# Optimization experiments

Measured on AMD Instinct MI355X. Metric: run time of the kernel, lower is better.

The kernel has to match this reference:

```python
import jax, jax.numpy as jnp
import numpy as np

NEG_BIG = -9e15
ALPHA = 0.2  # leakyrelu slope


def setup_inputs() -> dict:
    key = jax.random.key(0)
    k1, k2, k3, k4 = jax.random.split(key, 4)
    N, Fin, Fout = 8192, 256, 256
    input = jax.random.normal(k1, (N, Fin), dtype=jnp.float32)
    adj = jax.random.randint(k2, (N, N), 0, 2, dtype=jnp.int32)
    W = jax.random.normal(k3, (Fin, Fout), dtype=jnp.float32) * (1.0 / np.sqrt(Fin))
    a = jax.random.normal(k4, (2 * Fout, 1), dtype=jnp.float32) * (1.0 / np.sqrt(Fout))
    return {"input": input, "adj": adj, "W": W, "a": a}


def reference(input, adj, W, a):
    # h: [N, F]
    h = input @ W
    Fout = h.shape[1]
    # Fused score: e_ij = leakyrelu(h_i . a[:F] + h_j . a[F:])
    s1 = h @ a[:Fout, 0]   # [N]
    s2 = h @ a[Fout:, 0]   # [N]
    e = s1[:, None] + s2[None, :]            # [N, N]
    e = jnp.where(e >= 0, e, ALPHA * e)      # leaky relu
    e = jnp.where(adj > 0, e, NEG_BIG)       # mask
    attention = jax.nn.softmax(e, axis=1)    # row softmax
    h_prime = attention @ h                  # [N, F]
    return jax.nn.elu(h_prime)               # concat=True -> elu
```

## Files before the change

### kernel.cpp

```cpp
#include <hip/hip_runtime.h>
#include <hip/hip_bf16.h>

#define LRALPHA 0.2f

typedef __attribute__((ext_vector_type(8))) short frag_ab;
typedef __attribute__((ext_vector_type(4))) float frag_cd;
typedef int   iv4 __attribute__((ext_vector_type(4)));
typedef float fv4 __attribute__((ext_vector_type(4)));
typedef unsigned int uv4 __attribute__((ext_vector_type(4)));

static __device__ __forceinline__ unsigned short f2bf(float f) {
  __hip_bfloat16 b = __float2bfloat16(f);
  unsigned short u;
  __builtin_memcpy(&u, &b, 2);
  return u;
}

static __device__ __forceinline__ uv4 make_w(const iv4* ca, const fv4* cv,
                                             float s1r, float mr, float& zloc) {
  alignas(16) unsigned short wv[8];
#pragma unroll
  for (int g = 0; g < 2; ++g) {
#pragma unroll
    for (int e = 0; e < 4; ++e) {
      float ee = s1r + cv[g][e];
      ee = fmaxf(ee, LRALPHA * ee);
      float w = __expf(ee - mr);
      w = ca[g][e] ? w : 0.f;
      unsigned b = __float_as_uint(w);
      b += 0x7FFFu + ((b >> 16) & 1u);
      const unsigned short u = (unsigned short)(b >> 16);
      wv[g * 4 + e] = u;
      zloc += __uint_as_float((unsigned)u << 16);
    }
  }
  return *(const uv4*)wv;
}

__global__ __launch_bounds__(256, 4) void gat_hproj(
    const float* __restrict__ X, const float* __restrict__ W,
    const float* __restrict__ avec,
    float* __restrict__ s1, float* __restrict__ s2,
    unsigned short* __restrict__ hT) {
  const int tid = threadIdx.x;
  const int row0 = blockIdx.x * 16;
  const float* Xb = X + (size_t)row0 * 256;
  const int c = tid;

  float acc[16];
#pragma unroll
  for (int r = 0; r < 16; ++r) acc[r] = 0.f;

  for (int k = 0; k < 256; k += 4) {
    const float w0 = W[(k + 0) * 256 + c];
    const float w1 = W[(k + 1) * 256 + c];
    const float w2 = W[(k + 2) * 256 + c];
    const float w3 = W[(k + 3) * 256 + c];
#pragma unroll
    for (int r = 0; r < 16; ++r) {
      acc[r] = fmaf(Xb[r * 256 + k + 0], w0, acc[r]);
      acc[r] = fmaf(Xb[r * 256 + k + 1], w1, acc[r]);
      acc[r] = fmaf(Xb[r * 256 + k + 2], w2, acc[r]);
      acc[r] = fmaf(Xb[r * 256 + k + 3], w3, acc[r]);
    }
  }

  alignas(16) unsigned short hu[16];
#pragma unroll
  for (int r = 0; r < 16; ++r) hu[r] = f2bf(acc[r]);
  uv4* hdst = (uv4*)(hT + (size_t)c * 8192 + row0);
  hdst[0] = *(const uv4*)&hu[0];
  hdst[1] = *(const uv4*)&hu[8];

  const float a1c = avec[c];
  const float a2c = avec[256 + c];
  const int lane = tid & 63, wave = tid >> 6;
  __shared__ float r1[4][16], r2[4][16];
#pragma unroll
  for (int r = 0; r < 16; ++r) {
    float v1 = acc[r] * a1c;
    float v2 = acc[r] * a2c;
#pragma unroll
    for (int off = 32; off > 0; off >>= 1) {
      v1 += __shfl_down(v1, off);
      v2 += __shfl_down(v2, off);
    }
    if (lane == 0) { r1[wave][r] = v1; r2[wave][r] = v2; }
  }
  __syncthreads();
  if (tid < 16) {
    s1[row0 + tid] = r1[0][tid] + r1[1][tid] + r1[2][tid] + r1[3][tid];
    s2[row0 + tid] = r2[0][tid] + r2[1][tid] + r2[2][tid] + r2[3][tid];
  }
}

__global__ void gat_s2max(const float* __restrict__ s2, float* __restrict__ s2max) {
  const int tid = threadIdx.x;
  float m = -1e30f;
  for (int i = tid; i < 8192; i += 256) m = fmaxf(m, s2[i]);
#pragma unroll
  for (int off = 32; off > 0; off >>= 1) m = fmaxf(m, __shfl_down(m, off));
  __shared__ float ws[4];
  if ((tid & 63) == 0) ws[tid >> 6] = m;
  __syncthreads();
  if (tid == 0) s2max[0] = fmaxf(fmaxf(ws[0], ws[1]), fmaxf(ws[2], ws[3]));
}

__global__ __launch_bounds__(512, 4) void gat_attn(
    const int* __restrict__ adj, const unsigned short* __restrict__ hT,
    const float* __restrict__ s1, const float* __restrict__ s2,
    const float* __restrict__ s2maxp,
    float* __restrict__ pacc, float* __restrict__ pZ) {
  const int bid = blockIdx.x;
  const int x = bid & 7;
  const int ks = x >> 1;
  const int rb = ((bid >> 3) << 1) | (x & 1);
  const int row0 = rb * 64;
  const int jlo = ks * 2048;
  const int tid = threadIdx.x;
  const int wave = tid >> 6, lane = tid & 63;
  const int ln16 = lane & 15, quad = lane >> 4;

  __shared__ __align__(16) unsigned short P[2][64][72];
  __shared__ float Zred[64][8];

  const int r = tid >> 3, cq = tid & 7;
  const float s1r = s1[row0 + r];
  const float s2m = s2maxp[0];
  const float tmv = s1r + s2m;
  const float mr = tmv >= 0.f ? tmv : LRALPHA * tmv;

  const int* adjRow = adj + (size_t)(row0 + r) * 8192 + jlo + cq * 8;
  const float* s2p = s2 + jlo + cq * 8;

  frag_cd acc[4][2];
  const frag_cd fz = {0.f, 0.f, 0.f, 0.f};
#pragma unroll
  for (int mi = 0; mi < 4; ++mi)
#pragma unroll
    for (int ni = 0; ni < 2; ++ni) acc[mi][ni] = fz;

  float zloc = 0.f;
  const int NIT = 2048 / 64;

  {
    iv4 ca[2]; fv4 cv[2];
    ca[0] = __builtin_nontemporal_load((const iv4*)(adjRow));
    ca[1] = __builtin_nontemporal_load((const iv4*)(adjRow + 4));
    cv[0] = *(const fv4*)(s2p);
    cv[1] = *(const fv4*)(s2p + 4);
    *(uv4*)&P[0][r][cq * 8] = make_w(ca, cv, s1r, mr, zloc);
  }
  iv4 a[2]; fv4 v[2];
  a[0] = __builtin_nontemporal_load((const iv4*)(adjRow + 64));
  a[1] = __builtin_nontemporal_load((const iv4*)(adjRow + 68));
  v[0] = *(const fv4*)(s2p + 64);
  v[1] = *(const fv4*)(s2p + 68);
  __syncthreads();

  for (int jt = 0; jt < NIT; ++jt) {
    const int cur = jt & 1, nxt = cur ^ 1;
    const size_t jbase = (size_t)(jlo + jt * 64);

    frag_ab bf[2][2];
#pragma unroll
    for (int kk = 0; kk < 2; ++kk)
#pragma unroll
      for (int ni = 0; ni < 2; ++ni) {
        const int f = wave * 32 + ni * 16 + ln16;
        bf[kk][ni] = *(const frag_ab*)(hT + (size_t)f * 8192 + jbase + kk * 32 + quad * 8);
      }

    iv4 a2[2]; fv4 v2[2];
    if (jt + 2 < NIT) {
      const int o = (jt + 2) * 64;
      a2[0] = __builtin_nontemporal_load((const iv4*)(adjRow + o));
      a2[1] = __builtin_nontemporal_load((const iv4*)(adjRow + o + 4));
      v2[0] = *(const fv4*)(s2p + o);
      v2[1] = *(const fv4*)(s2p + o + 4);
    }

    if (jt + 1 < NIT) {
      *(uv4*)&P[nxt][r][cq * 8] = make_w(a, v, s1r, mr, zloc);
    }

#pragma unroll
    for (int kk = 0; kk < 2; ++kk) {
      frag_ab af[4];
#pragma unroll
      for (int mi = 0; mi < 4; ++mi)
        af[mi] = *(const frag_ab*)&P[cur][mi * 16 + ln16][kk * 32 + quad * 8];
#pragma unroll
      for (int mi = 0; mi < 4; ++mi)
#pragma unroll
        for (int ni = 0; ni < 2; ++ni)
          acc[mi][ni] = __builtin_amdgcn_mfma_f32_16x16x32_bf16(
              af[mi], bf[kk][ni], acc[mi][ni], 0, 0, 0);
    }
    __syncthreads();
    a[0] = a2[0]; a[1] = a2[1]; v[0] = v2[0]; v[1] = v2[1];
  }

  Zred[r][cq] = zloc;
  __syncthreads();
  if (tid < 64) {
    float z = 0.f;
#pragma unroll
    for (int q = 0; q < 8; ++q) z += Zred[tid][q];
    pZ[ks * 8192 + row0 + tid] = z;
  }

  float* paccb = pacc + ((size_t)ks * 8192 + row0) * 256;
#pragma unroll
  for (int mi = 0; mi < 4; ++mi) {
#pragma unroll
    for (int ni = 0; ni < 2; ++ni) {
      const int f = wave * 32 + ni * 16 + ln16;
#pragma unroll
      for (int reg = 0; reg < 4; ++reg) {
        const int grow = mi * 16 + quad * 4 + reg;
        __builtin_nontemporal_store(acc[mi][ni][reg], paccb + (size_t)grow * 256 + f);
      }
    }
  }
}

__global__ __launch_bounds__(256) void gat_combine(
    const float* __restrict__ pacc, const float* __restrict__ pZ,
    float* __restrict__ out) {
  const int idx = blockIdx.x * 256 + threadIdx.x;
  const int row = idx >> 6;
  const float z = pZ[row] + pZ[8192 + row] + pZ[16384 + row] + pZ[24576 + row];
  const float invz = 1.f / z;
  const size_t PSTRIDE = (size_t)8192 * 256;
  const fv4 n0 = *(const fv4*)(pacc + (size_t)idx * 4);
  const fv4 n1 = *(const fv4*)(pacc + PSTRIDE + (size_t)idx * 4);
  const fv4 n2 = *(const fv4*)(pacc + 2 * PSTRIDE + (size_t)idx * 4);
  const fv4 n3 = *(const fv4*)(pacc + 3 * PSTRIDE + (size_t)idx * 4);
  fv4 o;
#pragma unroll
  for (int e = 0; e < 4; ++e) {
    const float vsum = (n0[e] + n1[e]) + (n2[e] + n3[e]);
    const float vv = vsum * invz;
    o[e] = vv > 0.f ? vv : expm1f(vv);
  }
  *(fv4*)(out + (size_t)idx * 4) = o;
}

extern "C" void kernel_launch(void* const* d_in, const int* in_sizes, int n_in,
                              void* d_out, int out_size, void* d_ws, size_t ws_size,
                              hipStream_t stream) {
  const float* X = (const float*)d_in[0];
  const int* adj = (const int*)d_in[1];
  const float* W = (const float*)d_in[2];
  const float* avec = (const float*)d_in[3];
  float* out = (float*)d_out;

  float* wsf = (float*)d_ws;
  float* s1 = wsf;
  float* s2 = wsf + 8192;
  float* s2m = wsf + 16384;
  float* pZ = wsf + 24576;
  float* pacc = wsf + 65536;
  unsigned short* hT = (unsigned short*)(wsf + 65536 + 4 * 8192 * 256);

  hipLaunchKernelGGL(gat_hproj, dim3(512), dim3(256), 0, stream, X, W, avec, s1, s2, hT);
  hipLaunchKernelGGL(gat_s2max, dim3(1), dim3(256), 0, stream, s2, s2m);
  hipLaunchKernelGGL(gat_attn, dim3(512), dim3(512), 0, stream, adj, hT, s1, s2, s2m, pacc, pZ);
  hipLaunchKernelGGL(gat_combine, dim3(2048), dim3(256), 0, stream, pacc, pZ, out);
}
```

Measured before the change: 487.0 us.

## Fuse s2 max into projection via atomicMax and streamline softmax weight computation

Drops the separate single-block s2max kernel. The projection kernel now publishes each block's s2 maximum through an order-preserving unsigned key and atomicMax. The attention weight generation switches to exp2 with log2e-prescaled constants and packs bf16 by truncation using v_perm instead of round-to-nearest. The projection GEMM uses packed float2 FMAs, and s2 loads move later to cut live registers. Risks: the atomic key is never reset, so it relies on the workspace's initial or stale contents, and truncation changes the rounding of the attention weights.

```diff
diff --git a/kernel.cpp b/kernel.cpp
--- a/kernel.cpp
+++ b/kernel.cpp
@@ -2,11 +2,13 @@
 #include <hip/hip_bf16.h>
 
 #define LRALPHA 0.2f
+#define LOG2E 1.4426950408889634f
 
 typedef __attribute__((ext_vector_type(8))) short frag_ab;
 typedef __attribute__((ext_vector_type(4))) float frag_cd;
 typedef int   iv4 __attribute__((ext_vector_type(4)));
 typedef float fv4 __attribute__((ext_vector_type(4)));
+typedef float fv2 __attribute__((ext_vector_type(2)));
 typedef unsigned int uv4 __attribute__((ext_vector_type(4)));
 
 static __device__ __forceinline__ unsigned short f2bf(float f) {
@@ -17,57 +19,65 @@
 }
 
 static __device__ __forceinline__ uv4 make_w(const iv4* ca, const fv4* cv,
-                                             float s1r, float mr, float& zloc) {
-  alignas(16) unsigned short wv[8];
+                                             float c1, float c2, float& zloc) {
+  uv4 out;
 #pragma unroll
   for (int g = 0; g < 2; ++g) {
 #pragma unroll
-    for (int e = 0; e < 4; ++e) {
-      float ee = s1r + cv[g][e];
-      ee = fmaxf(ee, LRALPHA * ee);
-      float w = __expf(ee - mr);
-      w = ca[g][e] ? w : 0.f;
-      unsigned b = __float_as_uint(w);
-      b += 0x7FFFu + ((b >> 16) & 1u);
-      const unsigned short u = (unsigned short)(b >> 16);
-      wv[g * 4 + e] = u;
-      zloc += __uint_as_float((unsigned)u << 16);
-    }
-  }
-  return *(const uv4*)wv;
+    for (int h = 0; h < 2; ++h) {
+      unsigned b0, b1;
+#pragma unroll
+      for (int e = 0; e < 2; ++e) {
+        const int idx = h * 2 + e;
+        const float u = fmaf(cv[g][idx], LOG2E, c1);
+        const float m = fmaxf(u, LRALPHA * u);
+        float w = exp2f(m - c2);
+        w = ca[g][idx] ? w : 0.f;
+        const unsigned bb = __float_as_uint(w);
+        zloc += __uint_as_float(bb & 0xFFFF0000u);
+        if (e == 0) b0 = bb; else b1 = bb;
+      }
+      out[g * 2 + h] = __builtin_amdgcn_perm(b1, b0, 0x07060302u);
+    }
+  }
+  return out;
 }
 
 __global__ __launch_bounds__(256, 4) void gat_hproj(
     const float* __restrict__ X, const float* __restrict__ W,
     const float* __restrict__ avec,
     float* __restrict__ s1, float* __restrict__ s2,
+    unsigned* __restrict__ s2key,
     unsigned short* __restrict__ hT) {
   const int tid = threadIdx.x;
   const int row0 = blockIdx.x * 16;
   const float* Xb = X + (size_t)row0 * 256;
   const int c = tid;
 
-  float acc[16];
-#pragma unroll
-  for (int r = 0; r < 16; ++r) acc[r] = 0.f;
+  fv2 acc2[8];
+#pragma unroll
+  for (int p = 0; p < 8; ++p) acc2[p] = (fv2){0.f, 0.f};
 
   for (int k = 0; k < 256; k += 4) {
-    const float w0 = W[(k + 0) * 256 + c];
-    const float w1 = W[(k + 1) * 256 + c];
-    const float w2 = W[(k + 2) * 256 + c];
-    const float w3 = W[(k + 3) * 256 + c];
-#pragma unroll
-    for (int r = 0; r < 16; ++r) {
-      acc[r] = fmaf(Xb[r * 256 + k + 0], w0, acc[r]);
-      acc[r] = fmaf(Xb[r * 256 + k + 1], w1, acc[r]);
-      acc[r] = fmaf(Xb[r * 256 + k + 2], w2, acc[r]);
-      acc[r] = fmaf(Xb[r * 256 + k + 3], w3, acc[r]);
+    float wq[4];
+#pragma unroll
+    for (int i = 0; i < 4; ++i) wq[i] = W[(k + i) * 256 + c];
+#pragma unroll
+    for (int p = 0; p < 8; ++p) {
+      const float* xr0 = Xb + (2 * p) * 256 + k;
+      const float* xr1 = Xb + (2 * p + 1) * 256 + k;
+#pragma unroll
+      for (int i = 0; i < 4; ++i) {
+        const fv2 xv = {xr0[i], xr1[i]};
+        const fv2 wv = {wq[i], wq[i]};
+        acc2[p] += xv * wv;
+      }
     }
   }
 
   alignas(16) unsigned short hu[16];
 #pragma unroll
-  for (int r = 0; r < 16; ++r) hu[r] = f2bf(acc[r]);
+  for (int r = 0; r < 16; ++r) hu[r] = f2bf(acc2[r >> 1][r & 1]);
   uv4* hdst = (uv4*)(hT + (size_t)c * 8192 + row0);
   hdst[0] = *(const uv4*)&hu[0];
   hdst[1] = *(const uv4*)&hu[8];
@@ -78,8 +88,9 @@
   __shared__ float r1[4][16], r2[4][16];
 #pragma unroll
   for (int r = 0; r < 16; ++r) {
-    float v1 = acc[r] * a1c;
-    float v2 = acc[r] * a2c;
+    const float av = acc2[r >> 1][r & 1];
+    float v1 = av * a1c;
+    float v2 = av * a2c;
 #pragma unroll
     for (int off = 32; off > 0; off >>= 1) {
       v1 += __shfl_down(v1, off);
@@ -89,27 +100,25 @@
   }
   __syncthreads();
   if (tid < 16) {
-    s1[row0 + tid] = r1[0][tid] + r1[1][tid] + r1[2][tid] + r1[3][tid];
-    s2[row0 + tid] = r2[0][tid] + r2[1][tid] + r2[2][tid] + r2[3][tid];
-  }
-}
-
-__global__ void gat_s2max(const float* __restrict__ s2, float* __restrict__ s2max) {
-  const int tid = threadIdx.x;
-  float m = -1e30f;
-  for (int i = tid; i < 8192; i += 256) m = fmaxf(m, s2[i]);
-#pragma unroll
-  for (int off = 32; off > 0; off >>= 1) m = fmaxf(m, __shfl_down(m, off));
-  __shared__ float ws[4];
-  if ((tid & 63) == 0) ws[tid >> 6] = m;
-  __syncthreads();
-  if (tid == 0) s2max[0] = fmaxf(fmaxf(ws[0], ws[1]), fmaxf(ws[2], ws[3]));
+    const float v1 = r1[0][tid] + r1[1][tid] + r1[2][tid] + r1[3][tid];
+    const float v2 = r2[0][tid] + r2[1][tid] + r2[2][tid] + r2[3][tid];
+    s1[row0 + tid] = v1;
+    s2[row0 + tid] = v2;
+    float m = v2;
+#pragma unroll
+    for (int off = 8; off > 0; off >>= 1) m = fmaxf(m, __shfl_down(m, off));
+    if (tid == 0) {
+      const unsigned bits = __float_as_uint(m);
+      const unsigned key = bits ^ ((unsigned)((int)bits >> 31) | 0x80000000u);
+      atomicMax(s2key, key);
+    }
+  }
 }
 
 __global__ __launch_bounds__(512, 4) void gat_attn(
     const int* __restrict__ adj, const unsigned short* __restrict__ hT,
     const float* __restrict__ s1, const float* __restrict__ s2,
-    const float* __restrict__ s2maxp,
+    const unsigned* __restrict__ s2keyp,
     float* __restrict__ pacc, float* __restrict__ pZ) {
   const int bid = blockIdx.x;
   const int x = bid & 7;
@@ -126,9 +135,13 @@
 
   const int r = tid >> 3, cq = tid & 7;
   const float s1r = s1[row0 + r];
-  const float s2m = s2maxp[0];
+  const unsigned key = s2keyp[0];
+  const unsigned mb = (key & 0x80000000u) ? (key ^ 0x80000000u) : ~key;
+  const float s2m = __uint_as_float(mb);
   const float tmv = s1r + s2m;
-  const float mr = tmv >= 0.f ? tmv : LRALPHA * tmv;
+  const float mr = fmaxf(tmv, LRALPHA * tmv);
+  const float c1 = s1r * LOG2E;
+  const float c2 = mr * LOG2E;
 
   const int* adjRow = adj + (size_t)(row0 + r) * 8192 + jlo + cq * 8;
   const float* s2p = s2 + jlo + cq * 8;
@@ -149,13 +162,11 @@
     ca[1] = __builtin_nontemporal_load((const iv4*)(adjRow + 4));
     cv[0] = *(const fv4*)(s2p);
     cv[1] = *(const fv4*)(s2p + 4);
-    *(uv4*)&P[0][r][cq * 8] = make_w(ca, cv, s1r, mr, zloc);
-  }
-  iv4 a[2]; fv4 v[2];
+    *(uv4*)&P[0][r][cq * 8] = make_w(ca, cv, c1, c2, zloc);
+  }
+  iv4 a[2];
   a[0] = __builtin_nontemporal_load((const iv4*)(adjRow + 64));
   a[1] = __builtin_nontemporal_load((const iv4*)(adjRow + 68));
-  v[0] = *(const fv4*)(s2p + 64);
-  v[1] = *(const fv4*)(s2p + 68);
   __syncthreads();
 
   for (int jt = 0; jt < NIT; ++jt) {
@@ -171,17 +182,19 @@
         bf[kk][ni] = *(const frag_ab*)(hT + (size_t)f * 8192 + jbase + kk * 32 + quad * 8);
       }
 
-    iv4 a2[2]; fv4 v2[2];
+    iv4 a2[2];
     if (jt + 2 < NIT) {
       const int o = (jt + 2) * 64;
       a2[0] = __builtin_nontemporal_load((const iv4*)(adjRow + o));
       a2[1] = __builtin_nontemporal_load((const iv4*)(adjRow + o + 4));
-      v2[0] = *(const fv4*)(s2p + o);
-      v2[1] = *(const fv4*)(s2p + o + 4);
     }
 
     if (jt + 1 < NIT) {
-      *(uv4*)&P[nxt][r][cq * 8] = make_w(a, v, s1r, mr, zloc);
+      const int o = (jt + 1) * 64;
+      fv4 cv[2];
+      cv[0] = *(const fv4*)(s2p + o);
+      cv[1] = *(const fv4*)(s2p + o + 4);
+      *(uv4*)&P[nxt][r][cq * 8] = make_w(a, cv, c1, c2, zloc);
     }
 
 #pragma unroll
@@ -198,7 +211,7 @@
               af[mi], bf[kk][ni], acc[mi][ni], 0, 0, 0);
     }
     __syncthreads();
-    a[0] = a2[0]; a[1] = a2[1]; v[0] = v2[0]; v[1] = v2[1];
+    a[0] = a2[0]; a[1] = a2[1];
   }
 
   Zred[r][cq] = zloc;
@@ -259,13 +272,12 @@
   float* wsf = (float*)d_ws;
   float* s1 = wsf;
   float* s2 = wsf + 8192;
-  float* s2m = wsf + 16384;
+  unsigned* s2key = (unsigned*)(wsf + 16384);
   float* pZ = wsf + 24576;
   float* pacc = wsf + 65536;
   unsigned short* hT = (unsigned short*)(wsf + 65536 + 4 * 8192 * 256);
 
-  hipLaunchKernelGGL(gat_hproj, dim3(512), dim3(256), 0, stream, X, W, avec, s1, s2, hT);
-  hipLaunchKernelGGL(gat_s2max, dim3(1), dim3(256), 0, stream, s2, s2m);
-  hipLaunchKernelGGL(gat_attn, dim3(512), dim3(512), 0, stream, adj, hT, s1, s2, s2m, pacc, pZ);
+  hipLaunchKernelGGL(gat_hproj, dim3(512), dim3(256), 0, stream, X, W, avec, s1, s2, s2key, hT);
+  hipLaunchKernelGGL(gat_attn, dim3(512), dim3(512), 0, stream, adj, hT, s1, s2, s2key, pacc, pZ);
   hipLaunchKernelGGL(gat_combine, dim3(2048), dim3(256), 0, stream, pacc, pZ, out);
 }
```

Measured after the change: 489.4 us. About the same (+0.5%).
